# Kernel tuning notes

Measured on AMD Instinct MI355X. Metric: run time of the kernel, lower is better.

The kernel has to match this reference:

```python
import jax, jax.numpy as jnp
import numpy as np

B, D, R = 4096, 1024, 256
DT = 0.01
DT_SCALE = 1.0

# Yoshida 4th-order coefficients
_W1 = 1.0 / (2.0 - 2.0 ** (1.0 / 3.0))
_W0 = -(2.0 ** (1.0 / 3.0)) / (2.0 - 2.0 ** (1.0 / 3.0))
C1 = _W1 / 2.0
C2 = (_W0 + _W1) / 2.0
C3 = C2
C4 = C1
D1 = _W1
D2 = _W0
D3 = _W1


def setup_inputs() -> dict:
    key = jax.random.key(0)
    k1, k2, k3, k4, k5 = jax.random.split(key, 5)
    x = jax.random.normal(k1, (B, D), dtype=jnp.float32)
    v = jax.random.normal(k2, (B, D), dtype=jnp.float32)
    force = jax.random.normal(k3, (B, D), dtype=jnp.float32)
    # low-rank christoffel factors, scaled for numerical stability
    U = jax.random.normal(k4, (R, D), dtype=jnp.float32) * (1.0 / np.sqrt(D))
    W = jax.random.normal(k5, (D, R), dtype=jnp.float32) * (1.0 / np.sqrt(R))
    return {"x": x, "v": v, "force": force, "U": U, "W": W}


def _christoffel(tv, tx, U, W):
    # Gamma(v) = W @ (U v)^2  (low-rank quadratic form; x unused, matching
    # the gfn yoshida_fused(U, W) signature)
    h = jnp.einsum("rd,bd->br", U, tv)  # [B, R]
    return jnp.einsum("dr,br->bd", W, h * h)  # [B, D]


def reference(x, v, force, U, W):
    dt = DT * DT_SCALE

    def acceleration(tx, tv):
        return -_christoffel(tv, tx, U, W) + force

    x1 = x + C1 * dt * v
    v1 = v + D1 * dt * acceleration(x1, v)
    x2 = x1 + C2 * dt * v1
    v2 = v1 + D2 * dt * acceleration(x2, v1)
    x3 = x2 + C3 * dt * v2
    v3 = v2 + D3 * dt * acceleration(x3, v2)
    x_final = x3 + C4 * dt * v3
    return (x_final, v3)
```

## Files before the change

### kernel.cpp

```cpp
#include <hip/hip_runtime.h>


#define BSZ 4096
#define DD 1024
#define RR 256
#define NCOPY 4
#define COPY_BYTES (512u * 1024u)

typedef unsigned char uchar;
typedef long long i64;
typedef __attribute__((ext_vector_type(2))) long i64x2;
typedef __attribute__((ext_vector_type(4))) float f32x4;
typedef __attribute__((ext_vector_type(4))) unsigned int uint4v;
typedef __attribute__((ext_vector_type(4))) _Float16 f16x4;

__device__ inline unsigned int f2q4(float a, float b, float c, float d) {
    int lo = __builtin_amdgcn_cvt_pk_fp8_f32(a, b, 0, false);
    int hi = __builtin_amdgcn_cvt_pk_fp8_f32(c, d, lo, true);
    return (unsigned int)hi;
}
__device__ inline uchar f2q1(float x) {
    return (uchar)(__builtin_amdgcn_cvt_pk_fp8_f32(x, x, 0, false) & 0xff);
}

__global__ __launch_bounds__(256) void pack_uw_kernel(
    const float* __restrict__ U, const float* __restrict__ W,
    uchar* __restrict__ ws)
{
    const int g = blockIdx.x * 256 + threadIdx.x;
    const float* src;
    size_t off;
    float sc;
    if (g < 16384) {
        const int l = g & 63, p = (g >> 6) & 15, nt = g >> 10;
        src = U + (size_t)(nt * 16 + (l & 15)) * DD + p * 64 + (l >> 4) * 8;
        off = ((size_t)nt << 14) + (p << 10) + (l << 4);
        sc = 8.0f;
    } else {
        const int g2 = g - 16384;
        const int l = g2 & 63, p = (g2 >> 6) & 3, dt_ = g2 >> 8;
        src = W + (size_t)(dt_ * 16 + (l & 15)) * RR + p * 64 + (l >> 4) * 8;
        off = (size_t)(256 * 1024) + ((size_t)dt_ << 12) + (p << 10) + (l << 4);
        sc = 16.0f;
    }
    const float4 x0 = *reinterpret_cast<const float4*>(src);
    const float4 x1 = *reinterpret_cast<const float4*>(src + 4);
    const float4 y0 = *reinterpret_cast<const float4*>(src + 32);
    const float4 y1 = *reinterpret_cast<const float4*>(src + 36);
    uint4v o;
    o.x = f2q4(sc * x0.x, sc * x0.y, sc * x0.z, sc * x0.w);
    o.y = f2q4(sc * x1.x, sc * x1.y, sc * x1.z, sc * x1.w);
    o.z = f2q4(sc * y0.x, sc * y0.y, sc * y0.z, sc * y0.w);
    o.w = f2q4(sc * y1.x, sc * y1.y, sc * y1.z, sc * y1.w);
    #pragma unroll
    for (int c = 0; c < NCOPY; ++c)
        *reinterpret_cast<uint4v*>(ws + (size_t)c * COPY_BYTES + off) = o;
}

__global__ __launch_bounds__(1024, 1) void yoshida_fused_kernel(
    const float* __restrict__ x_in,
    const float* __restrict__ v_in,
    const float* __restrict__ force,
    const uchar* __restrict__ ws,
    float* __restrict__ x_out,
    float* __restrict__ v_out)
{
    __shared__ __align__(16) uchar vS[16][1040];
    __shared__ __align__(16) uchar H2S[16][272];
    __shared__ __align__(16) _Float16 fS[16][1032];
    __shared__ __align__(16) float xaS[16][1028];

    const int tid = threadIdx.x;
    const int w = tid >> 6, l = tid & 63;
    const int m = l & 15, q = l >> 4;
    const int b0 = blockIdx.x * 16;
    const int d0 = w * 64;

    const uchar* base = ws + (size_t)((blockIdx.x >> 3) & (NCOPY - 1)) * COPY_BYTES;

    constexpr double CBRT2 = 1.2599210498948731647672106072782;
    constexpr double W1c = 1.0 / (2.0 - CBRT2);
    constexpr double W0c = -CBRT2 * W1c;
    constexpr double DTd = 0.01 * 1.0;
    const float dcoef[3] = {(float)(W1c * DTd), (float)(W0c * DTd), (float)(W1c * DTd)};
    const float xcoef[3] = {(float)((W0c + W1c) * 0.5), (float)((W0c + W1c) * 0.5),
                            (float)(W1c * 0.5)};
    const float c1  = (float)(W1c * 0.5);
    const float dtf = (float)DTd;

    const uchar* up = base + ((size_t)w << 14) + (l << 4);
    const uchar* wp = base + 256 * 1024 + ((size_t)(w * 4) << 12) + (l << 4);

    i64x2 wreg[4][4];
    #pragma unroll
    for (int t = 0; t < 4; ++t)
        #pragma unroll
        for (int p = 0; p < 4; ++p)
            wreg[t][p] = *reinterpret_cast<const i64x2*>(wp + (t << 12) + (p << 10));

    {
        const int row = tid >> 6;
        const int col = (tid & 63) * 16;
        const float* sp = v_in + (size_t)(b0 + row) * DD + col;
        const float4 f0 = *reinterpret_cast<const float4*>(sp);
        const float4 f1 = *reinterpret_cast<const float4*>(sp + 4);
        const float4 f2 = *reinterpret_cast<const float4*>(sp + 8);
        const float4 f3 = *reinterpret_cast<const float4*>(sp + 12);
        uint4v pk;
        pk.x = f2q4(f0.x, f0.y, f0.z, f0.w);
        pk.y = f2q4(f1.x, f1.y, f1.z, f1.w);
        pk.z = f2q4(f2.x, f2.y, f2.z, f2.w);
        pk.w = f2q4(f3.x, f3.y, f3.z, f3.w);
        *reinterpret_cast<uint4v*>(&vS[row][col]) = pk;
    }

    {
        const float* sp = force + (size_t)(b0 + w) * DD;
        #pragma unroll
        for (int c = 0; c < 4; ++c) {
            const float4 f = *reinterpret_cast<const float4*>(sp + l * 4 + c * 256);
            f16x4 h;
            h.x = (_Float16)f.x; h.y = (_Float16)f.y;
            h.z = (_Float16)f.z; h.w = (_Float16)f.w;
            *reinterpret_cast<f16x4*>(&fS[w][l * 4 + c * 256]) = h;
        }
    }

    float vreg[16];
    #pragma unroll
    for (int t = 0; t < 4; ++t)
        #pragma unroll
        for (int i = 0; i < 4; ++i)
            vreg[t * 4 + i] =
                v_in[(size_t)(b0 + q * 4 + i) * DD + d0 + t * 16 + m];

    i64x2 ub[2][2];
    ub[0][0] = *reinterpret_cast<const i64x2*>(up);
    ub[0][1] = *reinterpret_cast<const i64x2*>(up + 1024);

    float xreg[16];

    #pragma unroll
    for (int s = 0; s < 3; ++s) {
        __syncthreads();

        f32x4 a0 = {0.f, 0.f, 0.f, 0.f}, a1 = {0.f, 0.f, 0.f, 0.f};
        #pragma unroll
        for (int pb = 0; pb < 8; ++pb) {
            if (pb < 7) {
                ub[(pb + 1) & 1][0] = *reinterpret_cast<const i64x2*>(
                    up + (((pb + 1) * 2 + 0) << 10));
                ub[(pb + 1) & 1][1] = *reinterpret_cast<const i64x2*>(
                    up + (((pb + 1) * 2 + 1) << 10));
            } else if (s < 2) {
                ub[0][0] = *reinterpret_cast<const i64x2*>(up);
                ub[0][1] = *reinterpret_cast<const i64x2*>(up + 1024);
            }
            #pragma unroll
            for (int j = 0; j < 2; ++j) {
                const int p = pb * 2 + j;
                const i64 af0 = *reinterpret_cast<const i64*>(&vS[m][p * 64 + q * 8]);
                const i64 af1 = *reinterpret_cast<const i64*>(&vS[m][p * 64 + 32 + q * 8]);
                a0 = __builtin_amdgcn_mfma_f32_16x16x32_fp8_fp8(
                         af0, ub[pb & 1][j].x, a0, 0, 0, 0);
                a1 = __builtin_amdgcn_mfma_f32_16x16x32_fp8_fp8(
                         af1, ub[pb & 1][j].y, a1, 0, 0, 0);
            }
        }
        #pragma unroll
        for (int i = 0; i < 4; ++i) {
            const float h8 = a0[i] + a1[i];
            H2S[q * 4 + i][w * 16 + m] = f2q1(h8 * h8 * 0.015625f);
        }
        __syncthreads();

        if (s == 2) {
            #pragma unroll
            for (int t = 0; t < 4; ++t)
                #pragma unroll
                for (int i = 0; i < 4; ++i)
                    xreg[t * 4 + i] =
                        x_in[(size_t)(b0 + q * 4 + i) * DD + d0 + t * 16 + m];
        }

        f32x4 accB[4];
        #pragma unroll
        for (int t = 0; t < 4; ++t) accB[t] = (f32x4){0.f, 0.f, 0.f, 0.f};
        #pragma unroll
        for (int p = 0; p < 4; ++p) {
            const i64 ha0 = *reinterpret_cast<const i64*>(&H2S[m][p * 64 + q * 8]);
            const i64 ha1 = *reinterpret_cast<const i64*>(&H2S[m][p * 64 + 32 + q * 8]);
            #pragma unroll
            for (int t = 0; t < 4; ++t) {
                accB[t] = __builtin_amdgcn_mfma_f32_16x16x32_fp8_fp8(
                              ha0, wreg[t][p].x, accB[t], 0, 0, 0);
                accB[t] = __builtin_amdgcn_mfma_f32_16x16x32_fp8_fp8(
                              ha1, wreg[t][p].y, accB[t], 0, 0, 0);
            }
        }

        const float ddt = dcoef[s], cx = xcoef[s], gsc = dcoef[s] * 0.0625f;
        #pragma unroll
        for (int t = 0; t < 4; ++t)
            #pragma unroll
            for (int i = 0; i < 4; ++i) {
                const int r = q * 4 + i, c = d0 + t * 16 + m;
                const float ff = (float)fS[r][c];
                const float vold = vreg[t * 4 + i];
                const float vn = vold + ddt * ff - gsc * accB[t][i];
                vreg[t * 4 + i] = vn;
                if (s == 0) {
                    xaS[r][c] = c1 * vold + cx * vn;
                    vS[r][c] = f2q1(vn);
                } else if (s == 1) {
                    xaS[r][c] += cx * vn;
                    vS[r][c] = f2q1(vn);
                } else {
                    const float xa = xaS[r][c] + cx * vn;
                    const size_t g = (size_t)(b0 + r) * DD + c;
                    x_out[g] = xreg[t * 4 + i] + dtf * xa;
                    v_out[g] = vn;
                }
            }
    }
}

extern "C" void kernel_launch(void* const* d_in, const int* in_sizes, int n_in,
                              void* d_out, int out_size, void* d_ws, size_t ws_size,
                              hipStream_t stream) {
    const float* x     = (const float*)d_in[0];
    const float* v     = (const float*)d_in[1];
    const float* force = (const float*)d_in[2];
    const float* U     = (const float*)d_in[3];
    const float* W     = (const float*)d_in[4];

    float* x_out = (float*)d_out;
    float* v_out = x_out + (size_t)BSZ * DD;

    uchar* ws = (uchar*)d_ws;

    pack_uw_kernel<<<dim3(128), dim3(256), 0, stream>>>(U, W, ws);
    yoshida_fused_kernel<<<dim3(BSZ / 16), dim3(1024), 0, stream>>>(
        x, v, force, ws, x_out, v_out);
}
```

Measured before the change: 139.3 us.

## Stream W fragments per stage instead of holding them in registers

Removes the 16 persistent W-fragment registers and instead reloads W fragments from the packed workspace each stage, double-buffered across the four K-steps of the second GEMM. The U prefetch becomes a 4-deep rolling register queue, and the x load moves after the second GEMM. The min-blocks hint is dropped from launch bounds. The aim is to cut register pressure and deepen load latency hiding, at the cost of re-reading W from cache three times per block.

```diff
diff --git a/kernel.cpp b/kernel.cpp
--- a/kernel.cpp
+++ b/kernel.cpp
@@ -57,7 +57,7 @@
         *reinterpret_cast<uint4v*>(ws + (size_t)c * COPY_BYTES + off) = o;
 }
 
-__global__ __launch_bounds__(1024, 1) void yoshida_fused_kernel(
+__global__ __launch_bounds__(1024) void yoshida_fused_kernel(
     const float* __restrict__ x_in,
     const float* __restrict__ v_in,
     const float* __restrict__ force,
@@ -90,13 +90,6 @@
 
     const uchar* up = base + ((size_t)w << 14) + (l << 4);
     const uchar* wp = base + 256 * 1024 + ((size_t)(w * 4) << 12) + (l << 4);
-
-    i64x2 wreg[4][4];
-    #pragma unroll
-    for (int t = 0; t < 4; ++t)
-        #pragma unroll
-        for (int p = 0; p < 4; ++p)
-            wreg[t][p] = *reinterpret_cast<const i64x2*>(wp + (t << 12) + (p << 10));
 
     {
         const int row = tid >> 6;
@@ -134,11 +127,10 @@
             vreg[t * 4 + i] =
                 v_in[(size_t)(b0 + q * 4 + i) * DD + d0 + t * 16 + m];
 
-    i64x2 ub[2][2];
-    ub[0][0] = *reinterpret_cast<const i64x2*>(up);
-    ub[0][1] = *reinterpret_cast<const i64x2*>(up + 1024);
-
-    float xreg[16];
+    i64x2 ub[4];
+    #pragma unroll
+    for (int p = 0; p < 4; ++p)
+        ub[p] = *reinterpret_cast<const i64x2*>(up + (p << 10));
 
     #pragma unroll
     for (int s = 0; s < 3; ++s) {
@@ -146,34 +138,53 @@
 
         f32x4 a0 = {0.f, 0.f, 0.f, 0.f}, a1 = {0.f, 0.f, 0.f, 0.f};
         #pragma unroll
-        for (int pb = 0; pb < 8; ++pb) {
-            if (pb < 7) {
-                ub[(pb + 1) & 1][0] = *reinterpret_cast<const i64x2*>(
-                    up + (((pb + 1) * 2 + 0) << 10));
-                ub[(pb + 1) & 1][1] = *reinterpret_cast<const i64x2*>(
-                    up + (((pb + 1) * 2 + 1) << 10));
-            } else if (s < 2) {
-                ub[0][0] = *reinterpret_cast<const i64x2*>(up);
-                ub[0][1] = *reinterpret_cast<const i64x2*>(up + 1024);
-            }
-            #pragma unroll
-            for (int j = 0; j < 2; ++j) {
-                const int p = pb * 2 + j;
-                const i64 af0 = *reinterpret_cast<const i64*>(&vS[m][p * 64 + q * 8]);
-                const i64 af1 = *reinterpret_cast<const i64*>(&vS[m][p * 64 + 32 + q * 8]);
-                a0 = __builtin_amdgcn_mfma_f32_16x16x32_fp8_fp8(
-                         af0, ub[pb & 1][j].x, a0, 0, 0, 0);
-                a1 = __builtin_amdgcn_mfma_f32_16x16x32_fp8_fp8(
-                         af1, ub[pb & 1][j].y, a1, 0, 0, 0);
-            }
+        for (int p = 0; p < 16; ++p) {
+            i64x2 nxt;
+            if (p < 12)
+                nxt = *reinterpret_cast<const i64x2*>(up + ((p + 4) << 10));
+            const i64 af0 = *reinterpret_cast<const i64*>(&vS[m][p * 64 + q * 8]);
+            const i64 af1 = *reinterpret_cast<const i64*>(&vS[m][p * 64 + 32 + q * 8]);
+            a0 = __builtin_amdgcn_mfma_f32_16x16x32_fp8_fp8(af0, ub[p & 3].x, a0, 0, 0, 0);
+            a1 = __builtin_amdgcn_mfma_f32_16x16x32_fp8_fp8(af1, ub[p & 3].y, a1, 0, 0, 0);
+            if (p < 12)
+                ub[p & 3] = nxt;
         }
         #pragma unroll
         for (int i = 0; i < 4; ++i) {
             const float h8 = a0[i] + a1[i];
             H2S[q * 4 + i][w * 16 + m] = f2q1(h8 * h8 * 0.015625f);
         }
+
+        i64x2 wb[2][4];
+        #pragma unroll
+        for (int t = 0; t < 4; ++t)
+            wb[0][t] = *reinterpret_cast<const i64x2*>(wp + (t << 12));
+
         __syncthreads();
 
+        f32x4 accB[4];
+        #pragma unroll
+        for (int t = 0; t < 4; ++t) accB[t] = (f32x4){0.f, 0.f, 0.f, 0.f};
+        #pragma unroll
+        for (int p = 0; p < 4; ++p) {
+            if (p < 3) {
+                #pragma unroll
+                for (int t = 0; t < 4; ++t)
+                    wb[(p + 1) & 1][t] = *reinterpret_cast<const i64x2*>(
+                        wp + (t << 12) + ((p + 1) << 10));
+            }
+            const i64 ha0 = *reinterpret_cast<const i64*>(&H2S[m][p * 64 + q * 8]);
+            const i64 ha1 = *reinterpret_cast<const i64*>(&H2S[m][p * 64 + 32 + q * 8]);
+            #pragma unroll
+            for (int t = 0; t < 4; ++t) {
+                accB[t] = __builtin_amdgcn_mfma_f32_16x16x32_fp8_fp8(
+                              ha0, wb[p & 1][t].x, accB[t], 0, 0, 0);
+                accB[t] = __builtin_amdgcn_mfma_f32_16x16x32_fp8_fp8(
+                              ha1, wb[p & 1][t].y, accB[t], 0, 0, 0);
+            }
+        }
+
+        float xreg[16];
         if (s == 2) {
             #pragma unroll
             for (int t = 0; t < 4; ++t)
@@ -181,22 +192,6 @@
                 for (int i = 0; i < 4; ++i)
                     xreg[t * 4 + i] =
                         x_in[(size_t)(b0 + q * 4 + i) * DD + d0 + t * 16 + m];
-        }
-
-        f32x4 accB[4];
-        #pragma unroll
-        for (int t = 0; t < 4; ++t) accB[t] = (f32x4){0.f, 0.f, 0.f, 0.f};
-        #pragma unroll
-        for (int p = 0; p < 4; ++p) {
-            const i64 ha0 = *reinterpret_cast<const i64*>(&H2S[m][p * 64 + q * 8]);
-            const i64 ha1 = *reinterpret_cast<const i64*>(&H2S[m][p * 64 + 32 + q * 8]);
-            #pragma unroll
-            for (int t = 0; t < 4; ++t) {
-                accB[t] = __builtin_amdgcn_mfma_f32_16x16x32_fp8_fp8(
-                              ha0, wreg[t][p].x, accB[t], 0, 0, 0);
-                accB[t] = __builtin_amdgcn_mfma_f32_16x16x32_fp8_fp8(
-                              ha1, wreg[t][p].y, accB[t], 0, 0, 0);
-            }
         }
 
         const float ddt = dcoef[s], cx = xcoef[s], gsc = dcoef[s] * 0.0625f;
@@ -222,6 +217,12 @@
                     v_out[g] = vn;
                 }
             }
+
+        if (s < 2) {
+            #pragma unroll
+            for (int p = 0; p < 4; ++p)
+                ub[p] = *reinterpret_cast<const i64x2*>(up + (p << 10));
+        }
     }
 }
 
```

Measured after the change: 126.2 us. 1.1x faster.
